# Kernel optimization log

Measured on AMD Instinct MI355X. Metric: run time of the kernel, lower is better.

The kernel has to match this reference:

```python
import jax, jax.numpy as jnp
import numpy as np

INF = 1.0e6  # 'infinity' for squared EDT; max real value is ~3*128^2 ~ 5e4


def edt_1d_sq(f, axis):
    """One pass of Felzenszwalb separable squared EDT along `axis`.
    d[i] = min_j f[j] + (i - j)^2  (brute-force vectorized lower envelope)."""
    f = jnp.moveaxis(f, axis, -1)
    n = f.shape[-1]
    i = jnp.arange(n, dtype=f.dtype)
    sq = (i[:, None] - i[None, :]) ** 2  # (n, n)
    d = jnp.min(f[..., None, :] + sq, axis=-1)  # (..., n)
    return jnp.moveaxis(d, -1, axis)


def compute_fg_dtm(mask):
    """Euclidean distance transform of foreground (distance to nearest background),
    matching scipy.ndimage.distance_transform_edt applied per batch element on the
    (C, X, Y, Z) mask (C==1 so the channel axis pass is the identity).
    mask: bool (B, 1, X, Y, Z) -> float32 (B, 1, X, Y, Z)."""
    def per_b(m):
        g = jnp.where(m, jnp.float32(INF), jnp.float32(0.0))
        for ax in range(m.ndim):
            g = edt_1d_sq(g, ax)
        return jnp.sqrt(g)
    return jax.lax.map(per_b, mask)


def setup_inputs() -> dict:
    key = jax.random.key(0)
    k1, k2, k3 = jax.random.split(key, 3)
    B, C, X, Y, Z = 2, 2, 128, 128, 128
    return {
        "outputs": jax.random.normal(k1, (B, C, X, Y, Z), dtype=jnp.float32),
        "outputs_dist": jax.random.normal(k2, (B, C, X, Y, Z), dtype=jnp.float32) * 10.0,
        "y": jax.random.randint(k3, (B, 1, X, Y, Z), 0, 2),
        "distance_map_weight": 1.0,
    }


def reference(outputs, outputs_dist, y, distance_map_weight):
    n_pred_ch = outputs.shape[1]
    # MONAI one_hot: (B,1,X,Y,Z) int labels -> (B,C,X,Y,Z) float
    y1h = jnp.moveaxis(jax.nn.one_hot(y[:, 0], n_pred_ch, dtype=outputs.dtype), -1, 1)
    x = outputs[:, 1:]            # foreground logits (B, 1, X, Y, Z)
    t = y1h[:, 1:]                # foreground mask
    od = outputs_dist[:, 1:]
    gt_dis = compute_fg_dtm(t > 0.5)
    # BCE with logits (mean reduction), numerically stable
    loss_ce = jnp.mean(jnp.maximum(x, 0.0) - x * t + jnp.log1p(jnp.exp(-jnp.abs(x))))
    # dice loss, flattened per batch element
    N = x.shape[0]
    smooth = jnp.float32(1.0)
    p = jax.nn.sigmoid(x).reshape(N, -1)
    tf = t.reshape(N, -1)
    dice = (2.0 * jnp.sum(p * tf, axis=1) + smooth) / (jnp.sum(p, axis=1) + jnp.sum(tf, axis=1) + smooth)
    loss_dice = 1.0 - jnp.sum(dice) / N
    # weighted L1 on the distance head, masked by the foreground mask
    msum = jnp.sum(t)
    loss_dist = jnp.where(
        msum == 0,
        jnp.float32(0.0),
        jnp.sum(jnp.abs(od - gt_dis) * t) / jnp.maximum(msum, jnp.float32(1e-12)),
    )
    return loss_ce + loss_dice + distance_map_weight * loss_dist
```

## Files before the change

### kernel.cpp

```cpp
#include <hip/hip_runtime.h>
#include <math.h>

#define M_SPATIAL 2097152

__device__ __forceinline__ float wave_redf(float v) {
#pragma unroll
  for (int o = 32; o > 0; o >>= 1) v += __shfl_down(v, o, 64);
  return v;
}
__device__ __forceinline__ double wave_redd(double v) {
#pragma unroll
  for (int o = 32; o > 0; o >>= 1) v += __shfl_down(v, o, 64);
  return v;
}
__device__ __forceinline__ float min3f(float a, float b, float c) {
  float d;
  asm("v_min3_f32 %0, %1, %2, %3" : "=v"(d) : "v"(a), "v"(b), "v"(c));
  return d;
}


__global__ __launch_bounds__(256) void kAB(const int* __restrict__ y,
                                           const float* __restrict__ outputs,
                                           float* __restrict__ g,
                                           double* __restrict__ part) {
  int blk = blockIdx.x;
  int b  = blk >> 9;
  int yy = (blk >> 2) & 127;
  int zq = blk & 3;
  int t  = threadIdx.x;
  int c  = t >> 5;
  int zl = t & 31;
  int x0 = c * 16;
  size_t sp   = (size_t)yy * 128 + (size_t)zq * 32 + zl;
  size_t base = (size_t)b * M_SPATIAL + sp;
  const float* xc = outputs + (size_t)(b * 2 + 1) * M_SPATIAL;

  int yb[16];
  float xv[16];
#pragma unroll
  for (int k = 0; k < 16; ++k) yb[k] = y[base + (size_t)(x0 + k) * 16384];
#pragma unroll
  for (int k = 0; k < 16; ++k) xv[k] = xc[sp + (size_t)(x0 + k) * 16384];

  int lastE = -200, nextE = 400;
#pragma unroll
  for (int k = 0; k < 16; ++k) lastE = (yb[k] == 1) ? lastE : (x0 + k);
#pragma unroll
  for (int k = 15; k >= 0; --k) nextE = (yb[k] == 1) ? nextE : (x0 + k);

  __shared__ int lE[8][32];
  __shared__ int nE[8][32];
  lE[c][zl] = lastE;
  nE[c][zl] = nextE;
  __syncthreads();

  int carryL = -200, carryN = 400;
#pragma unroll
  for (int q = 0; q < 7; ++q) {
    if (q < c)     carryL = max(carryL, lE[q][zl]);
    if (q + 1 > c) carryN = min(carryN, nE[q + 1][zl]);
  }

  float yy2f = (float)(yy * yy);
  float hinf = 1000000.f + yy2f;

  int df[16];
  int ll = carryL;
#pragma unroll
  for (int k = 0; k < 16; ++k) {
    ll = (yb[k] == 1) ? ll : (x0 + k);
    df[k] = min(x0 + k - ll, 200);
  }
  float ov[16];
  int nn = carryN;
#pragma unroll
  for (int k = 15; k >= 0; --k) {
    nn = (yb[k] == 1) ? nn : (x0 + k);
    int m = min(df[k], min(nn - (x0 + k), 200));
    ov[k] = (m >= 128) ? hinf : ((float)(m * m) + yy2f);
  }
#pragma unroll
  for (int k = 0; k < 16; ++k) g[base + (size_t)(x0 + k) * 16384] = ov[k];

  float ce = 0.f, ps = 0.f, pts = 0.f, tsum = 0.f;
#pragma unroll
  for (int k = 0; k < 16; ++k) {
    float tt = (yb[k] == 1) ? 1.0f : 0.0f;
    float xx = xv[k];
    ce += fmaxf(xx, 0.0f) - xx * tt + log1pf(expf(-fabsf(xx)));
    float p = 1.0f / (1.0f + expf(-xx));
    ps += p; pts += p * tt; tsum += tt;
  }
  float r0 = wave_redf(ce), r1 = wave_redf(ps), r2 = wave_redf(pts), r3 = wave_redf(tsum);
  __shared__ float sm[4][4];
  int lane = t & 63, w = t >> 6;
  if (lane == 0) { sm[w][0] = r0; sm[w][1] = r1; sm[w][2] = r2; sm[w][3] = r3; }
  __syncthreads();
  if (t == 0) {
    part[blk]        = (double)(sm[0][0] + sm[1][0] + sm[2][0] + sm[3][0]);
    part[1024 + blk] = (double)(sm[0][1] + sm[1][1] + sm[2][1] + sm[3][1]);
    part[2048 + blk] = (double)(sm[0][2] + sm[1][2] + sm[2][2] + sm[3][2]);
    part[3072 + blk] = (double)(sm[0][3] + sm[1][3] + sm[2][3] + sm[3][3]);
  }
}

__global__ __launch_bounds__(256) void kC_edty(float* __restrict__ g) {
  __shared__ float hl[128 * 33];
  int blk = blockIdx.x;
  int b = blk >> 9, xx = (blk >> 2) & 127, zc = blk & 3;
  int t = threadIdx.x;
  size_t rb = (size_t)b * M_SPATIAL + (size_t)xx * 16384 + (size_t)zc * 32;

#pragma unroll
  for (int r = 0; r < 4; ++r) {
    int i4 = t + r * 256;
    int j = i4 >> 3, w = i4 & 7;
    float4 v = *(const float4*)(g + rb + (size_t)j * 128 + 4 * w);
    hl[j * 33 + 4 * w + 0] = v.x;
    hl[j * 33 + 4 * w + 1] = v.y;
    hl[j * 33 + 4 * w + 2] = v.z;
    hl[j * 33 + 4 * w + 3] = v.w;
  }
  __syncthreads();

  int zl = t & 31, ig = t >> 5;
  float best[16], mc[16];
#pragma unroll
  for (int k = 0; k < 16; ++k) {
    best[k] = 3.0e38f;
    mc[k] = -2.0f * (float)(ig * 16 + k);
  }
#pragma unroll 2
  for (int j = 0; j < 128; j += 2) {
    float h0 = hl[j * 33 + zl];
    float h1 = hl[(j + 1) * 33 + zl];
    float j0 = (float)j, j1 = (float)(j + 1);
#pragma unroll
    for (int k = 0; k < 16; ++k) {
      float v0 = fmaf(mc[k], j0, h0);
      float v1 = fmaf(mc[k], j1, h1);
      best[k] = min3f(v0, v1, best[k]);
    }
  }
  int gz = zc * 32 + zl;
  float zq = (float)(gz * gz);
  size_t ob = rb + zl;
#pragma unroll
  for (int k = 0; k < 16; ++k) {
    int i = ig * 16 + k;
    float dY = (float)(i * i) + best[k];
    g[ob + (size_t)i * 128] = dY + zq;
  }
}

__global__ __launch_bounds__(256) void kD_edtz_dist(const float* __restrict__ g,
                                                    const float* __restrict__ od,
                                                    double* __restrict__ part) {
  __shared__ float hl[128 * 33];
  __shared__ float sred[4];
  int blk = blockIdx.x;
  int b = blk >> 9, xx = (blk >> 2) & 127, yc = blk & 3;
  int t = threadIdx.x;
  size_t rb = (size_t)b * M_SPATIAL + (size_t)xx * 16384 + (size_t)yc * 4096;
  int yl = t & 31, ig = t >> 5;

  size_t odb = (size_t)(2 * b + 1) * M_SPATIAL + (size_t)xx * 16384 +
               (size_t)yc * 4096 + (size_t)yl * 128 + (size_t)ig * 16;
  const float4* o4 = (const float4*)(od + odb);
  float4 ov[4];
#pragma unroll
  for (int r = 0; r < 4; ++r) ov[r] = o4[r];

  const float4* h4 = (const float4*)(g + rb);
#pragma unroll
  for (int r = 0; r < 4; ++r) {
    int i4 = t + r * 256;
    float4 v = h4[i4];
    int flat = i4 * 4;
    int z = flat & 127, yw = flat >> 7;
    hl[(z + 0) * 33 + yw] = v.x;
    hl[(z + 1) * 33 + yw] = v.y;
    hl[(z + 2) * 33 + yw] = v.z;
    hl[(z + 3) * 33 + yw] = v.w;
  }
  __syncthreads();

  float best[16], mc[16];
#pragma unroll
  for (int k = 0; k < 16; ++k) {
    best[k] = 3.0e38f;
    mc[k] = -2.0f * (float)(ig * 16 + k);
  }
#pragma unroll 2
  for (int j = 0; j < 128; j += 2) {
    float h0 = hl[j * 33 + yl];
    float h1 = hl[(j + 1) * 33 + yl];
    float j0 = (float)j, j1 = (float)(j + 1);
#pragma unroll
    for (int k = 0; k < 16; ++k) {
      float v0 = fmaf(mc[k], j0, h0);
      float v1 = fmaf(mc[k], j1, h1);
      best[k] = min3f(v0, v1, best[k]);
    }
  }
  const float* of = (const float*)ov;
  float dist = 0.f;
#pragma unroll
  for (int k = 0; k < 16; ++k) {
    int i = ig * 16 + k;
    float dv = (float)(i * i) + best[k];
    if (dv > 0.f) dist += fabsf(of[k] - sqrtf(dv));
  }
  float r = wave_redf(dist);
  int lane = t & 63, w = t >> 6;
  if (lane == 0) sred[w] = r;
  __syncthreads();
  if (t == 0) part[4096 + blk] = (double)(sred[0] + sred[1] + sred[2] + sred[3]);
}

__global__ __launch_bounds__(256) void k_final(const double* __restrict__ part,
                                               const float* __restrict__ wptr,
                                               float* __restrict__ out) {
  int i = threadIdx.x;
  double ce  = part[i] + part[i + 256] + part[i + 512] + part[i + 768];
  double p0  = part[1024 + i] + part[1024 + i + 256];
  double p1  = part[1536 + i] + part[1536 + i + 256];
  double pt0 = part[2048 + i] + part[2048 + i + 256];
  double pt1 = part[2560 + i] + part[2560 + i + 256];
  double t0  = part[3072 + i] + part[3072 + i + 256];
  double t1  = part[3584 + i] + part[3584 + i + 256];
  double ds  = part[4096 + i] + part[4096 + i + 256] + part[4096 + i + 512] + part[4096 + i + 768];

  ce = wave_redd(ce); p0 = wave_redd(p0); p1 = wave_redd(p1);
  pt0 = wave_redd(pt0); pt1 = wave_redd(pt1);
  t0 = wave_redd(t0); t1 = wave_redd(t1); ds = wave_redd(ds);

  __shared__ double sm[4][8];
  int lane = threadIdx.x & 63, w = threadIdx.x >> 6;
  if (lane == 0) {
    sm[w][0] = ce; sm[w][1] = p0; sm[w][2] = p1; sm[w][3] = pt0;
    sm[w][4] = pt1; sm[w][5] = t0; sm[w][6] = t1; sm[w][7] = ds;
  }
  __syncthreads();
  if (threadIdx.x == 0) {
    double a[8];
    for (int q = 0; q < 8; ++q) a[q] = sm[0][q] + sm[1][q] + sm[2][q] + sm[3][q];
    double cem = a[0] / 4194304.0;
    double dice0 = (2.0 * a[3] + 1.0) / (a[1] + a[5] + 1.0);
    double dice1 = (2.0 * a[4] + 1.0) / (a[2] + a[6] + 1.0);
    double ldice = 1.0 - 0.5 * (dice0 + dice1);
    double msum = a[5] + a[6];
    double ldist = (msum == 0.0) ? 0.0 : a[7] / fmax(msum, 1e-12);
    out[0] = (float)(cem + ldice + (double)wptr[0] * ldist);
  }
}

extern "C" void kernel_launch(void* const* d_in, const int* in_sizes, int n_in,
                              void* d_out, int out_size, void* d_ws, size_t ws_size,
                              hipStream_t stream) {
  const float* outputs      = (const float*)d_in[0];
  const float* outputs_dist = (const float*)d_in[1];
  const int*   y            = (const int*)d_in[2];
  const float* wptr         = (const float*)d_in[3];
  float* out = (float*)d_out;

  double* part = (double*)d_ws;
  float* g = (float*)((char*)d_ws + 65536);

  kAB<<<1024, 256, 0, stream>>>(y, outputs, g, part);
  kC_edty<<<1024, 256, 0, stream>>>(g);
  kD_edtz_dist<<<1024, 256, 0, stream>>>(g, outputs_dist, part);
  k_final<<<1, 256, 0, stream>>>(part, wptr, out);
}
```

Before: 160.7 us.

## Search a local window in Y/Z EDT passes, falling back to full scan

The Y and Z lower-envelope passes now first scan only a 32-wide window of candidates around each thread's 16 outputs, using a padded shared tile filled with large sentinels. A wave-wide bound check confirms that every windowed minimum is provably exact. If any lane fails the check, the wave redoes the full 128-candidate scan. This targets the quadratic inner loop on inputs with dense background, at the cost of extra shared memory, a vote, and a full rescan for waves that fail.

```diff
diff --git a/kernel.cpp b/kernel.cpp
--- a/kernel.cpp
+++ b/kernel.cpp
@@ -106,36 +106,43 @@
 }
 
 __global__ __launch_bounds__(256) void kC_edty(float* __restrict__ g) {
-  __shared__ float hl[128 * 33];
+  __shared__ float hl[144 * 33];
   int blk = blockIdx.x;
   int b = blk >> 9, xx = (blk >> 2) & 127, zc = blk & 3;
   int t = threadIdx.x;
   size_t rb = (size_t)b * M_SPATIAL + (size_t)xx * 16384 + (size_t)zc * 32;
 
 #pragma unroll
+  for (int idx = t; idx < 264; idx += 256) {
+    hl[idx] = 1.0e9f;
+    hl[136 * 33 + idx] = 1.0e9f;
+  }
+#pragma unroll
   for (int r = 0; r < 4; ++r) {
     int i4 = t + r * 256;
     int j = i4 >> 3, w = i4 & 7;
     float4 v = *(const float4*)(g + rb + (size_t)j * 128 + 4 * w);
-    hl[j * 33 + 4 * w + 0] = v.x;
-    hl[j * 33 + 4 * w + 1] = v.y;
-    hl[j * 33 + 4 * w + 2] = v.z;
-    hl[j * 33 + 4 * w + 3] = v.w;
+    hl[(j + 8) * 33 + 4 * w + 0] = v.x;
+    hl[(j + 8) * 33 + 4 * w + 1] = v.y;
+    hl[(j + 8) * 33 + 4 * w + 2] = v.z;
+    hl[(j + 8) * 33 + 4 * w + 3] = v.w;
   }
   __syncthreads();
 
   int zl = t & 31, ig = t >> 5;
+  int ibase = ig * 16;
   float best[16], mc[16];
 #pragma unroll
   for (int k = 0; k < 16; ++k) {
     best[k] = 3.0e38f;
-    mc[k] = -2.0f * (float)(ig * 16 + k);
-  }
-#pragma unroll 2
-  for (int j = 0; j < 128; j += 2) {
-    float h0 = hl[j * 33 + zl];
-    float h1 = hl[(j + 1) * 33 + zl];
-    float j0 = (float)j, j1 = (float)(j + 1);
+    mc[k] = -2.0f * (float)(ibase + k);
+  }
+  float jb = (float)(ibase - 8);
+#pragma unroll 4
+  for (int p = 0; p < 16; ++p) {
+    float h0 = hl[(ibase + 2 * p) * 33 + zl];
+    float h1 = hl[(ibase + 2 * p + 1) * 33 + zl];
+    float j0 = jb + (float)(2 * p), j1 = jb + (float)(2 * p + 1);
 #pragma unroll
     for (int k = 0; k < 16; ++k) {
       float v0 = fmaf(mc[k], j0, h0);
@@ -143,35 +150,70 @@
       best[k] = min3f(v0, v1, best[k]);
     }
   }
+  float dv[16];
+  int ok = 1;
+#pragma unroll
+  for (int k = 0; k < 16; ++k) {
+    int i = ibase + k;
+    dv[k] = (float)(i * i) + best[k];
+    float bnd = (float)min((k + 9) * (k + 9), (24 - k) * (24 - k));
+    ok &= (dv[k] <= bnd);
+  }
+  if (!__all(ok)) {
+#pragma unroll
+    for (int k = 0; k < 16; ++k) best[k] = 3.0e38f;
+#pragma unroll 2
+    for (int j = 0; j < 128; j += 2) {
+      float h0 = hl[(j + 8) * 33 + zl];
+      float h1 = hl[(j + 9) * 33 + zl];
+      float j0 = (float)j, j1 = (float)(j + 1);
+#pragma unroll
+      for (int k = 0; k < 16; ++k) {
+        float v0 = fmaf(mc[k], j0, h0);
+        float v1 = fmaf(mc[k], j1, h1);
+        best[k] = min3f(v0, v1, best[k]);
+      }
+    }
+#pragma unroll
+    for (int k = 0; k < 16; ++k) {
+      int i = ibase + k;
+      dv[k] = (float)(i * i) + best[k];
+    }
+  }
   int gz = zc * 32 + zl;
   float zq = (float)(gz * gz);
   size_t ob = rb + zl;
 #pragma unroll
   for (int k = 0; k < 16; ++k) {
-    int i = ig * 16 + k;
-    float dY = (float)(i * i) + best[k];
-    g[ob + (size_t)i * 128] = dY + zq;
+    int i = ibase + k;
+    g[ob + (size_t)i * 128] = dv[k] + zq;
   }
 }
 
 __global__ __launch_bounds__(256) void kD_edtz_dist(const float* __restrict__ g,
                                                     const float* __restrict__ od,
                                                     double* __restrict__ part) {
-  __shared__ float hl[128 * 33];
+  __shared__ float hl[144 * 33];
   __shared__ float sred[4];
   int blk = blockIdx.x;
   int b = blk >> 9, xx = (blk >> 2) & 127, yc = blk & 3;
   int t = threadIdx.x;
   size_t rb = (size_t)b * M_SPATIAL + (size_t)xx * 16384 + (size_t)yc * 4096;
   int yl = t & 31, ig = t >> 5;
+  int ibase = ig * 16;
 
   size_t odb = (size_t)(2 * b + 1) * M_SPATIAL + (size_t)xx * 16384 +
-               (size_t)yc * 4096 + (size_t)yl * 128 + (size_t)ig * 16;
+               (size_t)yc * 4096 + (size_t)yl * 128 + (size_t)ibase;
   const float4* o4 = (const float4*)(od + odb);
   float4 ov[4];
 #pragma unroll
   for (int r = 0; r < 4; ++r) ov[r] = o4[r];
 
+#pragma unroll
+  for (int idx = t; idx < 264; idx += 256) {
+    hl[idx] = 1.0e9f;
+    hl[136 * 33 + idx] = 1.0e9f;
+  }
   const float4* h4 = (const float4*)(g + rb);
 #pragma unroll
   for (int r = 0; r < 4; ++r) {
@@ -179,10 +221,10 @@
     float4 v = h4[i4];
     int flat = i4 * 4;
     int z = flat & 127, yw = flat >> 7;
-    hl[(z + 0) * 33 + yw] = v.x;
-    hl[(z + 1) * 33 + yw] = v.y;
-    hl[(z + 2) * 33 + yw] = v.z;
-    hl[(z + 3) * 33 + yw] = v.w;
+    hl[(z + 8) * 33 + yw] = v.x;
+    hl[(z + 9) * 33 + yw] = v.y;
+    hl[(z + 10) * 33 + yw] = v.z;
+    hl[(z + 11) * 33 + yw] = v.w;
   }
   __syncthreads();
 
@@ -190,13 +232,14 @@
 #pragma unroll
   for (int k = 0; k < 16; ++k) {
     best[k] = 3.0e38f;
-    mc[k] = -2.0f * (float)(ig * 16 + k);
-  }
-#pragma unroll 2
-  for (int j = 0; j < 128; j += 2) {
-    float h0 = hl[j * 33 + yl];
-    float h1 = hl[(j + 1) * 33 + yl];
-    float j0 = (float)j, j1 = (float)(j + 1);
+    mc[k] = -2.0f * (float)(ibase + k);
+  }
+  float jb = (float)(ibase - 8);
+#pragma unroll 4
+  for (int p = 0; p < 16; ++p) {
+    float h0 = hl[(ibase + 2 * p) * 33 + yl];
+    float h1 = hl[(ibase + 2 * p + 1) * 33 + yl];
+    float j0 = jb + (float)(2 * p), j1 = jb + (float)(2 * p + 1);
 #pragma unroll
     for (int k = 0; k < 16; ++k) {
       float v0 = fmaf(mc[k], j0, h0);
@@ -204,13 +247,41 @@
       best[k] = min3f(v0, v1, best[k]);
     }
   }
+  float dv[16];
+  int ok = 1;
+#pragma unroll
+  for (int k = 0; k < 16; ++k) {
+    int i = ibase + k;
+    dv[k] = (float)(i * i) + best[k];
+    float bnd = (float)min((k + 9) * (k + 9), (24 - k) * (24 - k));
+    ok &= (dv[k] <= bnd);
+  }
+  if (!__all(ok)) {
+#pragma unroll
+    for (int k = 0; k < 16; ++k) best[k] = 3.0e38f;
+#pragma unroll 2
+    for (int j = 0; j < 128; j += 2) {
+      float h0 = hl[(j + 8) * 33 + yl];
+      float h1 = hl[(j + 9) * 33 + yl];
+      float j0 = (float)j, j1 = (float)(j + 1);
+#pragma unroll
+      for (int k = 0; k < 16; ++k) {
+        float v0 = fmaf(mc[k], j0, h0);
+        float v1 = fmaf(mc[k], j1, h1);
+        best[k] = min3f(v0, v1, best[k]);
+      }
+    }
+#pragma unroll
+    for (int k = 0; k < 16; ++k) {
+      int i = ibase + k;
+      dv[k] = (float)(i * i) + best[k];
+    }
+  }
   const float* of = (const float*)ov;
   float dist = 0.f;
 #pragma unroll
   for (int k = 0; k < 16; ++k) {
-    int i = ig * 16 + k;
-    float dv = (float)(i * i) + best[k];
-    if (dv > 0.f) dist += fabsf(of[k] - sqrtf(dv));
+    if (dv[k] > 0.f) dist += fabsf(of[k] - sqrtf(dv[k]));
   }
   float r = wave_redf(dist);
   int lane = t & 63, w = t >> 6;
```

Result: faster. 141.9 us (-11.7%).
